# Optimization experiments

Hardware: AMD Instinct MI355X
Metric: run time of the kernel (lower is better)

Reference implementation:

```python
import jax, jax.numpy as jnp
import numpy as np

EPS = 1e-12

def _layer_norm(x, g, b):
    mu = jnp.mean(x, axis=-1, keepdims=True)
    var = jnp.mean(jnp.square(x - mu), axis=-1, keepdims=True)
    return (x - mu) * jax.lax.rsqrt(var + EPS) * g + b

def setup_inputs() -> dict:
    key = jax.random.key(0)
    ks = jax.random.split(key, 16)
    B, S, D, H, F = 2, 2048, 1024, 16, 4096
    s = 0.02
    inp = {
        "x": jax.random.normal(ks[0], (B, S, D), jnp.float32),
        "Wq": jax.random.normal(ks[1], (D, D), jnp.float32) * s,
        "bq": jnp.zeros((D,), jnp.float32),
        "Wk": jax.random.normal(ks[2], (D, D), jnp.float32) * s,
        "bk": jnp.zeros((D,), jnp.float32),
        "Wv": jax.random.normal(ks[3], (D, D), jnp.float32) * s,
        "bv": jnp.zeros((D,), jnp.float32),
        "Wo": jax.random.normal(ks[4], (D, D), jnp.float32) * s,
        "bo": jnp.zeros((D,), jnp.float32),
        "ln1_g": jnp.ones((D,), jnp.float32),
        "ln1_b": jnp.zeros((D,), jnp.float32),
        "W1": jax.random.normal(ks[5], (D, F), jnp.float32) * s,
        "b1": jnp.zeros((F,), jnp.float32),
        "W2": jax.random.normal(ks[6], (F, D), jnp.float32) * s,
        "b2": jnp.zeros((D,), jnp.float32),
        "ln2_g": jnp.ones((D,), jnp.float32),
        "ln2_b": jnp.zeros((D,), jnp.float32),
    }
    return inp

def reference(x, Wq, bq, Wk, bk, Wv, bv, Wo, bo, ln1_g, ln1_b, W1, b1, W2, b2, ln2_g, ln2_b):
    B, S, D = x.shape
    H = 16
    hd = D // H
    # q/k/v projections -> (B, H, S, hd)
    def split_heads(t):
        return t.reshape(B, S, H, hd).transpose(0, 2, 1, 3)
    q = split_heads(x @ Wq + bq)
    k = split_heads(x @ Wk + bk)
    v = split_heads(x @ Wv + bv)
    # naive attention: QK^T / sqrt(hd), softmax, AV
    scores = jnp.einsum("bhqd,bhkd->bhqk", q, k) / jnp.sqrt(jnp.float32(hd))
    attn = jax.nn.softmax(scores, axis=-1)
    ctx = jnp.einsum("bhqk,bhkd->bhqd", attn, v)
    ctx = ctx.transpose(0, 2, 1, 3).reshape(B, S, D)
    attn_out = _layer_norm(ctx @ Wo + bo, ln1_g, ln1_b)
    # FFN: relu -> gelu (exact, matching torch default) -> fc2 + residual -> LN
    h = jax.nn.gelu(jax.nn.relu(attn_out @ W1 + b1), approximate=False)
    out = _layer_norm(h @ W2 + b2 + attn_out, ln2_g, ln2_b)
    return out
```

## Files before the change

kernel.cpp:

```cpp
#include <hip/hip_runtime.h>
#include <hip/hip_bf16.h>
#include <cstdint>
#include <cstddef>

typedef __attribute__((ext_vector_type(8))) short short8;
typedef __attribute__((ext_vector_type(4))) float f32x4;
typedef __attribute__((ext_vector_type(4))) unsigned short ushort4v;

#define GLL(gp, lp) __builtin_amdgcn_global_load_lds(                         \
    (const __attribute__((address_space(1))) void*)(gp),                      \
    (__attribute__((address_space(3))) void*)(lp), 16, 0, 0)

static __device__ __forceinline__ unsigned short f2bf(float f) {
    union { float f; uint32_t u; } v; v.f = f;
    uint32_t r = v.u + 0x7FFF + ((v.u >> 16) & 1);
    return (unsigned short)(r >> 16);
}
static __device__ __forceinline__ float bf2f(unsigned short u) {
    union { uint32_t u; float f; } v; v.u = (uint32_t)u << 16; return v.f;
}

__global__ void pre_all_kernel(
    const float* __restrict__ x,
    const float* __restrict__ Wq, const float* __restrict__ Wk,
    const float* __restrict__ Wv, const float* __restrict__ Wo,
    const float* __restrict__ W1, const float* __restrict__ W2,
    unsigned short* __restrict__ xb,
    unsigned short* __restrict__ WqkvT, unsigned short* __restrict__ WoT,
    unsigned short* __restrict__ W1T, unsigned short* __restrict__ W2T)
{
    const int bid = blockIdx.x;
    const int tx = threadIdx.x, ty = threadIdx.y;
    if (bid >= 12288) {
        const int tid = ty * 32 + tx;
        const size_t base = (size_t)(bid - 12288) * 2048 + tid * 8;
        float4 v0 = *reinterpret_cast<const float4*>(x + base);
        float4 v1 = *reinterpret_cast<const float4*>(x + base + 4);
        unsigned short* d = xb + base;
        d[0] = f2bf(v0.x); d[1] = f2bf(v0.y); d[2] = f2bf(v0.z); d[3] = f2bf(v0.w);
        d[4] = f2bf(v1.x); d[5] = f2bf(v1.y); d[6] = f2bf(v1.z); d[7] = f2bf(v1.w);
        return;
    }
    __shared__ float tile[32][33];
    const float* src; unsigned short* dst; int K, N, local;
    if (bid < 4096) {
        int seg = bid >> 10; local = bid & 1023; K = 1024; N = 1024;
        src = (seg == 0) ? Wq : (seg == 1) ? Wk : (seg == 2) ? Wv : Wo;
        dst = (seg < 3) ? WqkvT + (size_t)seg * 1024 * 1024 : WoT;
    } else if (bid < 8192) {
        local = bid - 4096; K = 1024; N = 4096; src = W1; dst = W1T;
    } else {
        local = bid - 8192; K = 4096; N = 1024; src = W2; dst = W2T;
    }
    const int ntx = N >> 5;
    const int n0 = (local % ntx) * 32, k0 = (local / ntx) * 32;
#pragma unroll
    for (int j = 0; j < 32; j += 8)
        tile[ty + j][tx] = src[(size_t)(k0 + ty + j) * N + n0 + tx];
    __syncthreads();
#pragma unroll
    for (int j = 0; j < 32; j += 8)
        dst[(size_t)(n0 + ty + j) * K + k0 + tx] = f2bf(tile[tx][ty + j]);
}

template <int EPI>
__global__ __launch_bounds__(256) void gemm128_kernel(
    const unsigned short* __restrict__ A, const unsigned short* __restrict__ BT,
    int M, int N, int ld, int Kslice,
    const float* __restrict__ bias0, const float* __restrict__ bias1,
    const float* __restrict__ bias2,
    void* __restrict__ out0, void* __restrict__ out1, void* __restrict__ out2)
{
    __shared__ unsigned short Asm[2][128 * 64];
    __shared__ unsigned short Bsm[2][128 * 64];

    const int t = threadIdx.x;
    const int lane = t & 63, wv = t >> 6;
    const int wr = wv >> 1, wc = wv & 1;

    const int gx = gridDim.x;
    const int nwg = gx * gridDim.y;
    const int id = blockIdx.y * gx + blockIdx.x;
    const int swz = (id & 7) * (nwg >> 3) + (id >> 3);
    const int rowBase = (swz / gx) * 128;
    const int colBase = (swz % gx) * 128;
    const int koff = blockIdx.z * Kslice;

    const int r0 = t >> 3, c0 = t & 7;
    const int cg = c0 ^ (r0 & 7);
    const unsigned short* gA = A + (size_t)(rowBase + r0) * ld + koff + cg * 8;
    const unsigned short* gB = BT + (size_t)(colBase + r0) * ld + koff + cg * 8;

    auto stage = [&](int buf, int kt) {
#pragma unroll
        for (int j = 0; j < 4; j++) {
            GLL(gA + (size_t)(32 * j) * ld + kt, &Asm[buf][t * 8 + 2048 * j]);
            GLL(gB + (size_t)(32 * j) * ld + kt, &Bsm[buf][t * 8 + 2048 * j]);
        }
    };

    int aoff[4][2], boff[4][2];
#pragma unroll
    for (int m = 0; m < 4; m++)
#pragma unroll
        for (int ks = 0; ks < 2; ks++) {
            int rl = wr * 64 + m * 16 + (lane & 15);
            aoff[m][ks] = rl * 64 + (((ks * 4 + (lane >> 4)) ^ (rl & 7)) << 3);
            int cl = wc * 64 + m * 16 + (lane & 15);
            boff[m][ks] = cl * 64 + (((ks * 4 + (lane >> 4)) ^ (cl & 7)) << 3);
        }

    f32x4 acc[4][4];
#pragma unroll
    for (int m = 0; m < 4; m++)
#pragma unroll
        for (int n = 0; n < 4; n++) acc[m][n] = (f32x4){0.f, 0.f, 0.f, 0.f};

    stage(0, 0);
    asm volatile("s_waitcnt vmcnt(0)" ::: "memory");
    __builtin_amdgcn_s_barrier();

    const int nt = Kslice >> 6;
    for (int tt = 0; tt < nt; ++tt) {
        const int cur = tt & 1;
        if (tt + 1 < nt) stage(cur ^ 1, (tt + 1) << 6);

        short8 b[4][2];
#pragma unroll
        for (int n = 0; n < 4; n++)
#pragma unroll
            for (int ks = 0; ks < 2; ks++)
                b[n][ks] = *(const short8*)&Bsm[cur][boff[n][ks]];
        __builtin_amdgcn_s_setprio(1);
#pragma unroll
        for (int m = 0; m < 4; m++) {
            short8 a0 = *(const short8*)&Asm[cur][aoff[m][0]];
            short8 a1 = *(const short8*)&Asm[cur][aoff[m][1]];
#pragma unroll
            for (int n = 0; n < 4; n++) {
                acc[m][n] = __builtin_amdgcn_mfma_f32_16x16x32_bf16(
                    a0, b[n][0], acc[m][n], 0, 0, 0);
                acc[m][n] = __builtin_amdgcn_mfma_f32_16x16x32_bf16(
                    a1, b[n][1], acc[m][n], 0, 0, 0);
            }
        }
        __builtin_amdgcn_s_setprio(0);

        asm volatile("s_waitcnt vmcnt(0)" ::: "memory");
        __builtin_amdgcn_sched_barrier(0);
        __builtin_amdgcn_s_barrier();
    }

#pragma unroll
    for (int m = 0; m < 4; m++) {
#pragma unroll
        for (int n = 0; n < 4; n++) {
            const int col = colBase + wc * 64 + n * 16 + (lane & 15);
#pragma unroll
            for (int i = 0; i < 4; i++) {
                const int row = rowBase + wr * 64 + m * 16 + (lane >> 4) * 4 + i;
                float v = acc[m][n][i];
                if (EPI == 0) {
                    const int bb = row >> 11, s = row & 2047;
                    if (col < 1024) {
                        float q = (v + bias0[col]) * 0.18033688011112042f;
                        int h = col >> 6, d = col & 63;
                        ((unsigned short*)out0)[((size_t)(bb * 16 + h) * 2048 + s) * 64 + d] = f2bf(q);
                    } else if (col < 2048) {
                        int cc = col - 1024;
                        float kv = v + bias1[cc];
                        int h = cc >> 6, d = cc & 63;
                        ((unsigned short*)out1)[((size_t)(bb * 16 + h) * 2048 + s) * 64 + d] = f2bf(kv);
                    } else {
                        int cc = col - 2048;
                        float vv = v + bias2[cc];
                        int h = cc >> 6, d = cc & 63;
                        ((unsigned short*)out2)[((size_t)(bb * 16 + h) * 64 + d) * 2048 + s] = f2bf(vv);
                    }
                } else {
                    ((unsigned short*)out0)[(size_t)blockIdx.z * M * N + (size_t)row * N + col]
                        = f2bf(v);
                }
            }
        }
    }
}

template <int EPI>
__global__ __launch_bounds__(512, 2) void gemm256_kernel(
    const unsigned short* __restrict__ A, const unsigned short* __restrict__ BT,
    int M, int N, int K,
    const float* __restrict__ bias0, void* __restrict__ out0)
{
    extern __shared__ unsigned short lds[];

    const int t = threadIdx.x, lane = t & 63, w = t >> 6;
    const int wm = w >> 2, wn = w & 3;

    const int gx = gridDim.x;
    const int nwg = gx * gridDim.y;
    const int id = blockIdx.y * gx + blockIdx.x;
    const int swz = (id & 7) * (nwg >> 3) + (id >> 3);
    const int rowBase = (swz / gx) * 256;
    const int colBase = (swz % gx) * 256;

    const int r0 = t >> 3, c0 = t & 7;
    const int cg = c0 ^ (r0 & 7);
    const unsigned short* gA = A + (size_t)(rowBase + r0) * K + cg * 8;
    const unsigned short* gB = BT + (size_t)(colBase + r0) * K + cg * 8;

    auto stage = [&](int buf, int kt) {
#pragma unroll
        for (int j = 0; j < 4; j++) {
            GLL(gA + (size_t)(64 * j) * K + kt, &lds[buf * 16384 + t * 8 + 4096 * j]);
            GLL(gB + (size_t)(64 * j) * K + kt, &lds[32768 + buf * 16384 + t * 8 + 4096 * j]);
        }
    };

    int aoff[8][2], boff[4][2];
#pragma unroll
    for (int mf = 0; mf < 8; mf++)
#pragma unroll
        for (int ks = 0; ks < 2; ks++) {
            int rl = wm * 128 + mf * 16 + (lane & 15);
            aoff[mf][ks] = rl * 64 + (((ks * 4 + (lane >> 4)) ^ (rl & 7)) << 3);
        }
#pragma unroll
    for (int nf = 0; nf < 4; nf++)
#pragma unroll
        for (int ks = 0; ks < 2; ks++) {
            int cl = wn * 64 + nf * 16 + (lane & 15);
            boff[nf][ks] = cl * 64 + (((ks * 4 + (lane >> 4)) ^ (cl & 7)) << 3);
        }

    f32x4 acc[8][4];
#pragma unroll
    for (int mf = 0; mf < 8; mf++)
#pragma unroll
        for (int nf = 0; nf < 4; nf++) acc[mf][nf] = (f32x4){0.f, 0.f, 0.f, 0.f};

    stage(0, 0);
    asm volatile("s_waitcnt vmcnt(0)" ::: "memory");
    __builtin_amdgcn_s_barrier();

    const int nt = K >> 6;
    for (int tt = 0; tt < nt; ++tt) {
        const int cur = tt & 1;
        const int ab = cur * 16384, bbase = 32768 + cur * 16384;
        if (tt + 1 < nt) stage(cur ^ 1, (tt + 1) << 6);

        short8 b[4][2];
#pragma unroll
        for (int nf = 0; nf < 4; nf++)
#pragma unroll
            for (int ks = 0; ks < 2; ks++)
                b[nf][ks] = *(const short8*)&lds[bbase + boff[nf][ks]];
        __builtin_amdgcn_s_setprio(1);
#pragma unroll
        for (int mf = 0; mf < 8; mf++) {
            short8 a0 = *(const short8*)&lds[ab + aoff[mf][0]];
            short8 a1 = *(const short8*)&lds[ab + aoff[mf][1]];
#pragma unroll
            for (int nf = 0; nf < 4; nf++) {
                acc[mf][nf] = __builtin_amdgcn_mfma_f32_16x16x32_bf16(
                    a0, b[nf][0], acc[mf][nf], 0, 0, 0);
                acc[mf][nf] = __builtin_amdgcn_mfma_f32_16x16x32_bf16(
                    a1, b[nf][1], acc[mf][nf], 0, 0, 0);
            }
        }
        __builtin_amdgcn_s_setprio(0);

        asm volatile("s_waitcnt vmcnt(0)" ::: "memory");
        __builtin_amdgcn_sched_barrier(0);
        __builtin_amdgcn_s_barrier();
    }

#pragma unroll
    for (int mf = 0; mf < 8; mf++) {
#pragma unroll
        for (int nf = 0; nf < 4; nf++) {
            const int col = colBase + wn * 64 + nf * 16 + (lane & 15);
#pragma unroll
            for (int i = 0; i < 4; i++) {
                const int row = rowBase + wm * 128 + mf * 16 + (lane >> 4) * 4 + i;
                float z = acc[mf][nf][i] + bias0[col];
                if (z > 0.f) {
                    float u = 0.7978845608f * (z + 0.044715f * z * z * z);
                    float e = __builtin_amdgcn_exp2f(u * 2.8853900817779268f);
                    z = z * (1.f - 1.f / (e + 1.f));
                } else z = 0.f;
                ((unsigned short*)out0)[(size_t)row * N + col] = f2bf(z);
            }
        }
    }
}

__global__ __launch_bounds__(512) void flash_attn_kernel(
    const unsigned short* __restrict__ Qb, const unsigned short* __restrict__ Kb,
    const unsigned short* __restrict__ VT, unsigned short* __restrict__ ctxb)
{
    __shared__ unsigned short Ksm[2][64 * 64];
    __shared__ unsigned short Vsm[2][64 * 64];
    __shared__ unsigned short Psm[8][16 * 64];

    const int bh = blockIdx.y;
    const int q0 = blockIdx.x * 128;
    const int t = threadIdx.x, lane = t & 63, wv = t >> 6;

    const unsigned short* Qg = Qb + (size_t)bh * 2048 * 64;
    const unsigned short* Kg = Kb + (size_t)bh * 2048 * 64;
    const unsigned short* Vg = VT + (size_t)bh * 64 * 2048;

    short8 qf[2];
    {
        int r = q0 + wv * 16 + (lane & 15);
        qf[0] = *(const short8*)&Qg[(size_t)r * 64 + ((lane >> 4) << 3)];
        qf[1] = *(const short8*)&Qg[(size_t)r * 64 + 32 + ((lane >> 4) << 3)];
    }

    short8 onesf;
#pragma unroll
    for (int j = 0; j < 8; j++) onesf[j] = (short)0x3F80;

    f32x4 o[4], lacc;
#pragma unroll
    for (int n = 0; n < 4; n++) o[n] = (f32x4){0.f, 0.f, 0.f, 0.f};
    lacc = (f32x4){0.f, 0.f, 0.f, 0.f};

    const int r0 = t >> 3, sl = t & 7;
    const int cg0 = sl ^ (r0 & 7);

    auto stageKV = [&](int buf, int kt) {
        GLL(&Kg[(size_t)(kt + r0) * 64 + cg0 * 8], &Ksm[buf][t * 8]);
        GLL(&Vg[(size_t)r0 * 2048 + kt + cg0 * 8], &Vsm[buf][t * 8]);
    };

    unsigned short* P = &Psm[wv][0];

    int pwaddr[4][4];
#pragma unroll
    for (int n = 0; n < 4; n++)
#pragma unroll
        for (int i = 0; i < 4; i++) {
            int rl = (lane >> 4) * 4 + i;
            int col = n * 16 + (lane & 15);
            pwaddr[n][i] = rl * 64 + ((((col >> 3) ^ (rl & 7)) << 3) | (col & 7));
        }

    stageKV(0, 0);
    asm volatile("s_waitcnt vmcnt(0)" ::: "memory");
    __builtin_amdgcn_s_barrier();

    for (int tt = 0; tt < 32; ++tt) {
        const int cur = tt & 1;
        if (tt + 1 < 32) stageKV(cur ^ 1, (tt + 1) << 6);

        f32x4 s[4];
        __builtin_amdgcn_s_setprio(1);
#pragma unroll
        for (int n = 0; n < 4; n++) {
            s[n] = (f32x4){0.f, 0.f, 0.f, 0.f};
            int rl = n * 16 + (lane & 15);
#pragma unroll
            for (int kb = 0; kb < 2; kb++) {
                int slot = ((kb << 2) + (lane >> 4)) ^ (rl & 7);
                short8 kf = *(const short8*)&Ksm[cur][rl * 64 + slot * 8];
                s[n] = __builtin_amdgcn_mfma_f32_16x16x32_bf16(qf[kb], kf, s[n], 0, 0, 0);
            }
        }
        __builtin_amdgcn_s_setprio(0);

#pragma unroll
        for (int n = 0; n < 4; n++)
#pragma unroll
            for (int i = 0; i < 4; i++) {
                float p = __builtin_amdgcn_exp2f(s[n][i]);
                union { float f; uint32_t u; } pv; pv.f = p;
                P[pwaddr[n][i]] = (unsigned short)(pv.u >> 16);
            }

        short8 pf[2];
        {
            int rl = lane & 15;
#pragma unroll
            for (int kb = 0; kb < 2; kb++) {
                int slot = ((kb << 2) + (lane >> 4)) ^ (rl & 7);
                pf[kb] = *(const short8*)&P[rl * 64 + slot * 8];
            }
        }
        __builtin_amdgcn_s_setprio(1);
        lacc = __builtin_amdgcn_mfma_f32_16x16x32_bf16(pf[0], onesf, lacc, 0, 0, 0);
        lacc = __builtin_amdgcn_mfma_f32_16x16x32_bf16(pf[1], onesf, lacc, 0, 0, 0);
#pragma unroll
        for (int n = 0; n < 4; n++) {
            int d = n * 16 + (lane & 15);
#pragma unroll
            for (int kb = 0; kb < 2; kb++) {
                int slot = ((kb << 2) + (lane >> 4)) ^ (d & 7);
                short8 vf = *(const short8*)&Vsm[cur][d * 64 + slot * 8];
                o[n] = __builtin_amdgcn_mfma_f32_16x16x32_bf16(pf[kb], vf, o[n], 0, 0, 0);
            }
        }
        __builtin_amdgcn_s_setprio(0);

        asm volatile("s_waitcnt vmcnt(0)" ::: "memory");
        __builtin_amdgcn_sched_barrier(0);
        __builtin_amdgcn_s_barrier();
    }

    const int bb = bh >> 4, h = bh & 15;
#pragma unroll
    for (int i = 0; i < 4; i++) {
        float linv = 1.f / lacc[i];
        int srow = q0 + wv * 16 + (lane >> 4) * 4 + i;
#pragma unroll
        for (int n = 0; n < 4; n++) {
            int d = n * 16 + (lane & 15);
            ctxb[((size_t)(bb * 2048 + srow)) * 1024 + h * 64 + d] =
                f2bf(o[n][i] * linv);
        }
    }
}

__global__ __launch_bounds__(256) void ln_kernel(
    const unsigned short* __restrict__ in0, const unsigned short* __restrict__ in1,
    const unsigned short* __restrict__ resid, const float* __restrict__ bias,
    const float* __restrict__ g, const float* __restrict__ bta,
    float* __restrict__ outf, unsigned short* __restrict__ outb)
{
    const int row = blockIdx.x;
    const int t = threadIdx.x, lane = t & 63, wv = t >> 6;
    const size_t base = (size_t)row * 1024 + t * 4;

    ushort4v u0 = *reinterpret_cast<const ushort4v*>(in0 + base);
    ushort4v u1 = *reinterpret_cast<const ushort4v*>(in1 + base);
    float4 xv;
    xv.x = bf2f(u0[0]) + bf2f(u1[0]);
    xv.y = bf2f(u0[1]) + bf2f(u1[1]);
    xv.z = bf2f(u0[2]) + bf2f(u1[2]);
    xv.w = bf2f(u0[3]) + bf2f(u1[3]);
    if (resid) {
        ushort4v ur = *reinterpret_cast<const ushort4v*>(resid + base);
        xv.x += bf2f(ur[0]); xv.y += bf2f(ur[1]);
        xv.z += bf2f(ur[2]); xv.w += bf2f(ur[3]);
    }
    {
        float4 bv = *reinterpret_cast<const float4*>(bias + t * 4);
        xv.x += bv.x; xv.y += bv.y; xv.z += bv.z; xv.w += bv.w;
    }

    float s = xv.x + xv.y + xv.z + xv.w;
    float ss = xv.x * xv.x + xv.y * xv.y + xv.z * xv.z + xv.w * xv.w;
#pragma unroll
    for (int off = 1; off < 64; off <<= 1) {
        s += __shfl_xor(s, off);
        ss += __shfl_xor(ss, off);
    }
    __shared__ float red[8];
    if (lane == 0) { red[wv] = s; red[4 + wv] = ss; }
    __syncthreads();
    s = red[0] + red[1] + red[2] + red[3];
    ss = red[4] + red[5] + red[6] + red[7];
    const float mu = s * (1.f / 1024.f);
    const float var = ss * (1.f / 1024.f) - mu * mu;
    const float inv = rsqrtf(var + 1e-12f);

    float4 gv = *reinterpret_cast<const float4*>(g + t * 4);
    float4 bv = *reinterpret_cast<const float4*>(bta + t * 4);
    float o0 = (xv.x - mu) * inv * gv.x + bv.x;
    float o1 = (xv.y - mu) * inv * gv.y + bv.y;
    float o2 = (xv.z - mu) * inv * gv.z + bv.z;
    float o3 = (xv.w - mu) * inv * gv.w + bv.w;

    if (outf)
        *reinterpret_cast<float4*>(outf + base) = (float4){o0, o1, o2, o3};
    if (outb) {
        unsigned short* ob = outb + base;
        ob[0] = f2bf(o0); ob[1] = f2bf(o1); ob[2] = f2bf(o2); ob[3] = f2bf(o3);
    }
}

extern "C" void kernel_launch(void* const* d_in, const int* in_sizes, int n_in,
                              void* d_out, int out_size, void* d_ws, size_t ws_size,
                              hipStream_t stream) {
    const float* x     = (const float*)d_in[0];
    const float* Wq    = (const float*)d_in[1];
    const float* bq    = (const float*)d_in[2];
    const float* Wk    = (const float*)d_in[3];
    const float* bk    = (const float*)d_in[4];
    const float* Wv    = (const float*)d_in[5];
    const float* bv    = (const float*)d_in[6];
    const float* Wo    = (const float*)d_in[7];
    const float* bo    = (const float*)d_in[8];
    const float* ln1_g = (const float*)d_in[9];
    const float* ln1_b = (const float*)d_in[10];
    const float* W1    = (const float*)d_in[11];
    const float* b1    = (const float*)d_in[12];
    const float* W2    = (const float*)d_in[13];
    const float* b2    = (const float*)d_in[14];
    const float* ln2_g = (const float*)d_in[15];
    const float* ln2_b = (const float*)d_in[16];
    float* out = (float*)d_out;

    const int B = 2, S = 2048, D = 1024, H = 16, F = 4096;
    const int M = B * S;

    char* w = (char*)d_ws;
    size_t off = 0;
    auto alloc = [&](size_t bytes) {
        size_t o = off; off += (bytes + 255) & ~(size_t)255; return o;
    };
    unsigned short* xb      = (unsigned short*)(w + alloc((size_t)M * D * 2));
    unsigned short* WqkvT   = (unsigned short*)(w + alloc((size_t)3 * D * D * 2));
    unsigned short* WoT     = (unsigned short*)(w + alloc((size_t)D * D * 2));
    unsigned short* W1T     = (unsigned short*)(w + alloc((size_t)D * F * 2));
    unsigned short* W2T     = (unsigned short*)(w + alloc((size_t)F * D * 2));
    unsigned short* Qbuf    = (unsigned short*)(w + alloc((size_t)M * D * 2));
    unsigned short* Kbuf    = (unsigned short*)(w + alloc((size_t)M * D * 2));
    unsigned short* VTbuf   = (unsigned short*)(w + alloc((size_t)M * D * 2));
    unsigned short* z0      = (unsigned short*)(w + alloc((size_t)M * D * 2));
    unsigned short* z1      = (unsigned short*)(w + alloc((size_t)M * D * 2));
    unsigned short* attnlnb = (unsigned short*)(w + alloc((size_t)M * D * 2));
    unsigned short* hbuf    = (unsigned short*)(w + alloc((size_t)M * F * 2));
    unsigned short* ctxb    = xb;

    hipFuncSetAttribute((const void*)gemm256_kernel<2>,
                        hipFuncAttributeMaxDynamicSharedMemorySize, 131072);

    pre_all_kernel<<<14336, dim3(32, 8), 0, stream>>>(
        x, Wq, Wk, Wv, Wo, W1, W2, xb, WqkvT, WoT, W1T, W2T);

    gemm128_kernel<0><<<dim3(3 * D / 128, M / 128, 1), 256, 0, stream>>>(
        xb, WqkvT, M, 3 * D, D, D, bq, bk, bv, Qbuf, Kbuf, VTbuf);

    flash_attn_kernel<<<dim3(S / 128, B * H), 512, 0, stream>>>(
        Qbuf, Kbuf, VTbuf, ctxb);

    gemm128_kernel<4><<<dim3(D / 128, M / 128, 2), 256, 0, stream>>>(
        ctxb, WoT, M, D, D, D / 2, nullptr, nullptr, nullptr, z0, nullptr, nullptr);

    ln_kernel<<<M, 256, 0, stream>>>(z0, z1, nullptr, bo, ln1_g, ln1_b,
                                     nullptr, attnlnb);

    gemm256_kernel<2><<<dim3(F / 256, M / 256), 512, 131072, stream>>>(
        attnlnb, W1T, M, F, D, b1, hbuf);

    gemm128_kernel<4><<<dim3(D / 128, M / 128, 2), 256, 0, stream>>>(
        hbuf, W2T, M, D, F, F / 2, nullptr, nullptr, nullptr, z0, nullptr, nullptr);

    ln_kernel<<<M, 256, 0, stream>>>(z0, z1, attnlnb, b2, ln2_g, ln2_b,
                                     out, nullptr);
}
```

Baseline: 240.3 us.

## Load GEMM A fragments directly from global into registers, keep only B in LDS

The 128x128 GEMM kernel stops staging the A tile through shared memory. Each wave now loads its A fragments straight from global memory into registers, double-buffered across an unrolled-by-two K loop, while B is still staged in LDS with global_load_lds. This halves LDS use and removes the A-side LDS reads, and launch bounds now request 3 blocks per SM to use that headroom. In exchange, each wave issues uncoalesced 16-byte global loads for A, and register pressure rises from two sets of A fragments, which could cause spills under the tighter occupancy bound.

After: 422.8 us. +75.9%, slower.

```diff
diff --git a/kernel.cpp b/kernel.cpp
--- a/kernel.cpp
+++ b/kernel.cpp
@@ -64,14 +64,13 @@
 }
 
 template <int EPI>
-__global__ __launch_bounds__(256) void gemm128_kernel(
+__global__ __launch_bounds__(256, 3) void gemm128_kernel(
     const unsigned short* __restrict__ A, const unsigned short* __restrict__ BT,
     int M, int N, int ld, int Kslice,
     const float* __restrict__ bias0, const float* __restrict__ bias1,
     const float* __restrict__ bias2,
     void* __restrict__ out0, void* __restrict__ out1, void* __restrict__ out2)
 {
-    __shared__ unsigned short Asm[2][128 * 64];
     __shared__ unsigned short Bsm[2][128 * 64];
 
     const int t = threadIdx.x;
@@ -88,67 +87,81 @@
 
     const int r0 = t >> 3, c0 = t & 7;
     const int cg = c0 ^ (r0 & 7);
-    const unsigned short* gA = A + (size_t)(rowBase + r0) * ld + koff + cg * 8;
     const unsigned short* gB = BT + (size_t)(colBase + r0) * ld + koff + cg * 8;
 
-    auto stage = [&](int buf, int kt) {
-#pragma unroll
-        for (int j = 0; j < 4; j++) {
-            GLL(gA + (size_t)(32 * j) * ld + kt, &Asm[buf][t * 8 + 2048 * j]);
+    auto stageB = [&](int buf, int kt) {
+#pragma unroll
+        for (int j = 0; j < 4; j++)
             GLL(gB + (size_t)(32 * j) * ld + kt, &Bsm[buf][t * 8 + 2048 * j]);
-        }
     };
 
-    int aoff[4][2], boff[4][2];
+    const unsigned short* gAfrag =
+        A + (size_t)(rowBase + wr * 64 + (lane & 15)) * ld + koff + ((lane >> 4) << 3);
+
+    auto loadA = [&](short8 (&a)[4][2], int kt) {
+#pragma unroll
+        for (int m = 0; m < 4; m++)
+#pragma unroll
+            for (int ks = 0; ks < 2; ks++)
+                a[m][ks] = *(const short8*)&gAfrag[(size_t)(m * 16) * ld + kt + ks * 32];
+    };
+
+    int boff[4][2];
+#pragma unroll
+    for (int n = 0; n < 4; n++)
+#pragma unroll
+        for (int ks = 0; ks < 2; ks++) {
+            int cl = wc * 64 + n * 16 + (lane & 15);
+            boff[n][ks] = cl * 64 + (((ks * 4 + (lane >> 4)) ^ (cl & 7)) << 3);
+        }
+
+    f32x4 acc[4][4];
 #pragma unroll
     for (int m = 0; m < 4; m++)
 #pragma unroll
-        for (int ks = 0; ks < 2; ks++) {
-            int rl = wr * 64 + m * 16 + (lane & 15);
-            aoff[m][ks] = rl * 64 + (((ks * 4 + (lane >> 4)) ^ (rl & 7)) << 3);
-            int cl = wc * 64 + m * 16 + (lane & 15);
-            boff[m][ks] = cl * 64 + (((ks * 4 + (lane >> 4)) ^ (cl & 7)) << 3);
-        }
-
-    f32x4 acc[4][4];
-#pragma unroll
-    for (int m = 0; m < 4; m++)
-#pragma unroll
         for (int n = 0; n < 4; n++) acc[m][n] = (f32x4){0.f, 0.f, 0.f, 0.f};
 
-    stage(0, 0);
+    auto compute = [&](short8 (&a)[4][2], int buf) {
+        short8 b[4][2];
+#pragma unroll
+        for (int n = 0; n < 4; n++)
+#pragma unroll
+            for (int ks = 0; ks < 2; ks++)
+                b[n][ks] = *(const short8*)&Bsm[buf][boff[n][ks]];
+        __builtin_amdgcn_s_setprio(1);
+#pragma unroll
+        for (int m = 0; m < 4; m++)
+#pragma unroll
+            for (int n = 0; n < 4; n++) {
+                acc[m][n] = __builtin_amdgcn_mfma_f32_16x16x32_bf16(
+                    a[m][0], b[n][0], acc[m][n], 0, 0, 0);
+                acc[m][n] = __builtin_amdgcn_mfma_f32_16x16x32_bf16(
+                    a[m][1], b[n][1], acc[m][n], 0, 0, 0);
+            }
+        __builtin_amdgcn_s_setprio(0);
+    };
+
+    short8 a0[4][2], a1[4][2];
+    stageB(0, 0);
+    loadA(a0, 0);
     asm volatile("s_waitcnt vmcnt(0)" ::: "memory");
     __builtin_amdgcn_s_barrier();
 
     const int nt = Kslice >> 6;
-    for (int tt = 0; tt < nt; ++tt) {
-        const int cur = tt & 1;
-        if (tt + 1 < nt) stage(cur ^ 1, (tt + 1) << 6);
-
-        short8 b[4][2];
-#pragma unroll
-        for (int n = 0; n < 4; n++)
-#pragma unroll
-            for (int ks = 0; ks < 2; ks++)
-                b[n][ks] = *(const short8*)&Bsm[cur][boff[n][ks]];
-        __builtin_amdgcn_s_setprio(1);
-#pragma unroll
-        for (int m = 0; m < 4; m++) {
-            short8 a0 = *(const short8*)&Asm[cur][aoff[m][0]];
-            short8 a1 = *(const short8*)&Asm[cur][aoff[m][1]];
-#pragma unroll
-            for (int n = 0; n < 4; n++) {
-                acc[m][n] = __builtin_amdgcn_mfma_f32_16x16x32_bf16(
-                    a0, b[n][0], acc[m][n], 0, 0, 0);
-                acc[m][n] = __builtin_amdgcn_mfma_f32_16x16x32_bf16(
-                    a1, b[n][1], acc[m][n], 0, 0, 0);
-            }
-        }
-        __builtin_amdgcn_s_setprio(0);
-
+    for (int tt = 0; tt < nt; tt += 2) {
+        const int kt1 = (tt + 1) << 6, kt2 = (tt + 2) << 6;
+        if (tt + 1 < nt) { stageB(1, kt1); loadA(a1, kt1); }
+        compute(a0, 0);
         asm volatile("s_waitcnt vmcnt(0)" ::: "memory");
         __builtin_amdgcn_sched_barrier(0);
         __builtin_amdgcn_s_barrier();
+        if (tt + 1 < nt) {
+            if (tt + 2 < nt) { stageB(0, kt2); loadA(a0, kt2); }
+            compute(a1, 1);
+            asm volatile("s_waitcnt vmcnt(0)" ::: "memory");
+            __builtin_amdgcn_sched_barrier(0);
+            __builtin_amdgcn_s_barrier();
+        }
     }
 
 #pragma unroll
```
